# Kernel optimization log

Hardware: AMD Instinct MI355X
Metric: run time of the kernel (lower is better)

## Reference

```python
import jax, jax.numpy as jnp
import numpy as np
import math

D_MODEL = 1024
N_HEAD = 16
D_FF = 4096
N_LAYERS = 4
SEQ = 2048
BATCH = 1
LN_EPS = 1e-5


def _pos_encoding(S, D, dtype):
    pos = jnp.arange(S, dtype=dtype)[:, None]                      # [S,1]
    div = jnp.exp(jnp.arange(0, D, 2, dtype=dtype) * (-math.log(10000.0) / D))
    ang = pos * div                                                 # [S,D/2]
    pe = jnp.stack([jnp.sin(ang), jnp.cos(ang)], axis=-1).reshape(S, D)  # interleave sin/cos
    return pe[:, None, :]                                           # [S,1,D]


def _layernorm(x, g, b):
    mu = jnp.mean(x, axis=-1, keepdims=True)
    var = jnp.mean(jnp.square(x - mu), axis=-1, keepdims=True)
    return (x - mu) * jax.lax.rsqrt(var + LN_EPS) * g + b


def setup_inputs() -> dict:
    key = jax.random.key(0)
    ks = jax.random.split(key, 16)
    f32 = jnp.float32
    L, D, F = N_LAYERS, D_MODEL, D_FF
    s = 0.02
    inp = {
        "X": jax.random.normal(ks[0], (SEQ, BATCH, D), dtype=f32),
        "Wqkv": jax.random.normal(ks[1], (L, 3 * D, D), dtype=f32) * s,
        "bqkv": jnp.zeros((L, 3 * D), dtype=f32),
        "Wo": jax.random.normal(ks[2], (L, D, D), dtype=f32) * s,
        "bo": jnp.zeros((L, D), dtype=f32),
        "ln1_g": jnp.ones((L, D), dtype=f32),
        "ln1_b": jnp.zeros((L, D), dtype=f32),
        "W1": jax.random.normal(ks[3], (L, F, D), dtype=f32) * s,
        "b1": jnp.zeros((L, F), dtype=f32),
        "W2": jax.random.normal(ks[4], (L, D, F), dtype=f32) * s,
        "b2": jnp.zeros((L, D), dtype=f32),
        "ln2_g": jnp.ones((L, D), dtype=f32),
        "ln2_b": jnp.zeros((L, D), dtype=f32),
        "Wdec": jax.random.normal(ks[5], (3, D), dtype=f32) * s,
        "bdec": jnp.zeros((3,), dtype=f32),
        "window_size": 128,
        "nhead": 16,
    }
    return inp


def reference(X, Wqkv, bqkv, Wo, bo, ln1_g, ln1_b, W1, b1, W2, b2, ln2_g, ln2_b, Wdec, bdec, window_size, nhead):
    S, B, D = X.shape
    H = nhead
    hd = D // H
    scale = 1.0 / math.sqrt(hd)

    x = X + _pos_encoding(S, D, X.dtype)  # dropout is identity at eval

    # banded additive mask: allowed iff |i-j| < window_size (triu/tril(-inf) construction)
    idx = jnp.arange(S)
    band = jnp.abs(idx[:, None] - idx[None, :]) < window_size
    mask = jnp.where(band, jnp.array(0.0, X.dtype), jnp.array(-jnp.inf, X.dtype))  # [S,S]

    L = Wqkv.shape[0]
    for l in range(L):
        # self-attention (post-norm encoder layer)
        qkv = jnp.einsum('sbd,ed->sbe', x, Wqkv[l]) + bqkv[l]
        q, k, v = jnp.split(qkv, 3, axis=-1)
        q = q.reshape(S, B, H, hd)
        k = k.reshape(S, B, H, hd)
        v = v.reshape(S, B, H, hd)
        scores = jnp.einsum('sbhd,tbhd->bhst', q, k) * scale + mask  # [B,H,S,S]
        attn = jax.nn.softmax(scores, axis=-1)
        o = jnp.einsum('bhst,tbhd->sbhd', attn, v).reshape(S, B, D)
        o = jnp.einsum('sbd,ed->sbe', o, Wo[l]) + bo[l]
        x = _layernorm(x + o, ln1_g[l], ln1_b[l])
        # feed-forward (relu)
        h = jax.nn.relu(jnp.einsum('sbd,fd->sbf', x, W1[l]) + b1[l])
        ff = jnp.einsum('sbf,df->sbd', h, W2[l]) + b2[l]
        x = _layernorm(x + ff, ln2_g[l], ln2_b[l])

    logits = jnp.einsum('sbd,cd->sbc', x, Wdec) + bdec  # [S,B,3]
    return jax.nn.log_softmax(logits, axis=-1)
```

## Files before the change

kernel.cpp:

```cpp
#include <hip/hip_runtime.h>
#include <hip/hip_bf16.h>
#include <cmath>

typedef __hip_bfloat16 bf16;
typedef __bf16 bf16x8 __attribute__((ext_vector_type(8)));
typedef float f32x4 __attribute__((ext_vector_type(4)));

typedef __attribute__((address_space(1))) void void_g;
typedef __attribute__((address_space(3))) void void_l;

#define SEQ 2048
#define DMODEL 1024
#define NHEAD 16
#define HDIM 64
#define DFF 4096
#define WINDOW 128
#define LN_EPS 1e-5f

__device__ __forceinline__ void gl_lds16(const bf16* g, bf16* l) {
    __builtin_amdgcn_global_load_lds((void_g*)(g), (void_l*)(l), 16, 0, 0);
}

__device__ __forceinline__ bf16x8 cvt8(float4 a, float4 b) {
    bf16x8 w;
    w[0] = (__bf16)a.x; w[1] = (__bf16)a.y; w[2] = (__bf16)a.z; w[3] = (__bf16)a.w;
    w[4] = (__bf16)b.x; w[5] = (__bf16)b.y; w[6] = (__bf16)b.z; w[7] = (__bf16)b.w;
    return w;
}

__global__ __launch_bounds__(256)
void add_pe(const float* __restrict__ X, bf16* __restrict__ x) {
    int idx = blockIdx.x * 256 + threadIdx.x;
    int s = idx >> 10, d = idx & 1023;
    float i2 = (float)(d & ~1);
    float div = expf(i2 * (-9.210340371976184f / 1024.0f));
    float ang = (float)s * div;
    float pe = (d & 1) ? cosf(ang) : sinf(ang);
    x[idx] = (bf16)(X[idx] + pe);
}

__global__ __launch_bounds__(256)
void cvt_w_layer(const float* __restrict__ wqkv, const float* __restrict__ wo,
                 const float* __restrict__ w1, const float* __restrict__ w2,
                 bf16* __restrict__ dst)
{
    int i = blockIdx.x * 256 + threadIdx.x;
    const float* src; size_t so;
    if (i < 393216)       { src = wqkv; so = (size_t)i * 8; }
    else if (i < 524288)  { src = wo;   so = (size_t)(i - 393216) * 8; }
    else if (i < 1048576) { src = w1;   so = (size_t)(i - 524288) * 8; }
    else                  { src = w2;   so = (size_t)(i - 1048576) * 8; }
    float4 a = *(const float4*)(src + so);
    float4 b = *(const float4*)(src + so + 4);
    *(bf16x8*)(dst + (size_t)i * 8) = cvt8(a, b);
}


#define G8_PROLOGUE(Adecl, Wdecl)                                                \
    __shared__ __align__(16) bf16 AS[3][256 * 64];                               \
    __shared__ __align__(16) bf16 BS[3][128 * 64];                               \
    const int tid  = threadIdx.x;                                                \
    const int lane = tid & 63;                                                   \
    const int wave = tid >> 6;                                                   \
    const int wm = wave >> 1, wn = wave & 1;                                     \
    const int r = lane & 15, quad = lane >> 4;                                   \
    const int rc = (quad ^ (r & 3)) * 8;                                         \
    f32x4 acc[4][4];                                                             \
    _Pragma("unroll")                                                            \
    for (int i = 0; i < 4; ++i)                                                  \
        _Pragma("unroll")                                                        \
        for (int j = 0; j < 4; ++j) acc[i][j] = (f32x4){0.f, 0.f, 0.f, 0.f};     \
    const bf16* ApA[4]; const bf16* ApB[2];                                      \
    _Pragma("unroll")                                                            \
    for (int i = 0; i < 4; ++i) {                                                \
        int c = tid + 512 * i;                                                   \
        int ks = c >> 10, row = (c >> 2) & 255, kch = (c & 3) ^ (row & 3);       \
        ApA[i] = (Adecl) + (size_t)(m0 + row) * K + ks * 32 + kch * 8;           \
    }                                                                            \
    _Pragma("unroll")                                                            \
    for (int i = 0; i < 2; ++i) {                                                \
        int c = tid + 512 * i;                                                   \
        int ks = c >> 9, row = (c >> 2) & 127, kch = (c & 3) ^ (row & 3);        \
        ApB[i] = (Wdecl) + (size_t)(n0 + row) * K + ks * 32 + kch * 8;           \
    }

#define G8_STAGE(koff, Adst, Bdst)                                               \
    _Pragma("unroll")                                                            \
    for (int i = 0; i < 4; ++i)                                                  \
        gl_lds16(ApA[i] + (koff), (Adst) + (size_t)(tid + 512 * i) * 8);         \
    _Pragma("unroll")                                                            \
    for (int i = 0; i < 2; ++i)                                                  \
        gl_lds16(ApB[i] + (koff), (Bdst) + (size_t)(tid + 512 * i) * 8);

#define G8_KLOOP(Klim)                                                           \
    const int nit = (Klim) / 64;                                                 \
    bf16 *A_c = &AS[0][0], *A_n = &AS[1][0], *A_f = &AS[2][0];                   \
    bf16 *B_c = &BS[0][0], *B_n = &BS[1][0], *B_f = &BS[2][0];                   \
    G8_STAGE(0, A_c, B_c)                                                        \
    if (nit > 1) {                                                               \
        G8_STAGE(64, A_n, B_n)                                                   \
        asm volatile("s_waitcnt vmcnt(6)" ::: "memory");                         \
    } else {                                                                     \
        asm volatile("s_waitcnt vmcnt(0)" ::: "memory");                         \
    }                                                                            \
    __builtin_amdgcn_s_barrier();                                                \
    for (int t = 0; t < nit; ++t) {                                              \
        const bool stg = (t + 2 < nit);                                          \
        if (stg) { G8_STAGE((t + 2) * 64, A_f, B_f) }                            \
        bf16x8 av[4][2], bv[4][2];                                               \
        _Pragma("unroll")                                                        \
        for (int mf = 0; mf < 4; ++mf)                                           \
            _Pragma("unroll")                                                    \
            for (int kk = 0; kk < 2; ++kk)                                       \
                av[mf][kk] = *(const bf16x8*)(A_c + kk * 8192 +                  \
                              (wm * 64 + mf * 16 + r) * 32 + rc);                \
        _Pragma("unroll")                                                        \
        for (int nf = 0; nf < 4; ++nf)                                           \
            _Pragma("unroll")                                                    \
            for (int kk = 0; kk < 2; ++kk)                                       \
                bv[nf][kk] = *(const bf16x8*)(B_c + kk * 4096 +                  \
                              (wn * 64 + nf * 16 + r) * 32 + rc);                \
        __builtin_amdgcn_s_setprio(1);                                           \
        _Pragma("unroll")                                                        \
        for (int mf = 0; mf < 4; ++mf)                                           \
            _Pragma("unroll")                                                    \
            for (int nf = 0; nf < 4; ++nf)                                       \
                _Pragma("unroll")                                                \
                for (int kk = 0; kk < 2; ++kk)                                   \
                    acc[mf][nf] = __builtin_amdgcn_mfma_f32_16x16x32_bf16(       \
                        av[mf][kk], bv[nf][kk], acc[mf][nf], 0, 0, 0);           \
        __builtin_amdgcn_s_setprio(0);                                           \
        if (stg) asm volatile("s_waitcnt vmcnt(6)" ::: "memory");                \
        else     asm volatile("s_waitcnt vmcnt(0)" ::: "memory");                \
        __builtin_amdgcn_s_barrier();                                            \
        bf16* tA = A_c; A_c = A_n; A_n = A_f; A_f = tA;                          \
        bf16* tB = B_c; B_c = B_n; B_n = B_f; B_f = tB;                          \
    }

#define G8_SWZ_TILE()                                                            \
    const int gx = gridDim.x, gy = gridDim.y;                                    \
    const int bid = blockIdx.y * gx + blockIdx.x;                                \
    const int cpx = (gx * gy) >> 3;                                              \
    const int swz = (bid & 7) * cpx + (bid >> 3);                                \
    const int m0 = (swz / gx) * 256, n0 = (swz % gx) * 128;

template<int ACT>
__global__ __launch_bounds__(512)
void gemm8_bt(const bf16* __restrict__ A, const bf16* __restrict__ W,
              const float* __restrict__ bias, bf16* __restrict__ C,
              int M, int N, int K)
{
    G8_SWZ_TILE()
    G8_PROLOGUE(A, W)
    G8_KLOOP(K)
#pragma unroll
    for (int nt = 0; nt < 4; ++nt) {
        int n = n0 + wn * 64 + nt * 16 + r;
        float bv = bias[n];
#pragma unroll
        for (int mt = 0; mt < 4; ++mt) {
#pragma unroll
            for (int e = 0; e < 4; ++e) {
                int m = m0 + wm * 64 + mt * 16 + quad * 4 + e;
                float v = acc[mt][nt][e] + bv;
                if (ACT == 1) v = fmaxf(v, 0.f);
                C[(size_t)m * N + n] = (bf16)v;
            }
        }
    }
}

template<int SPLIT>
__global__ __launch_bounds__(512)
void gemm8_splitk(const bf16* __restrict__ A, const bf16* __restrict__ Wfull,
                  float* __restrict__ Cacc, int M, int N, int K)
{
    G8_SWZ_TILE()
    const int Kc = K / SPLIT;
    const bf16* Ab = A + (size_t)blockIdx.z * Kc;
    const bf16* W = Wfull + (size_t)blockIdx.z * Kc;
    float* Cz = Cacc + (size_t)blockIdx.z * M * N;
    G8_PROLOGUE(Ab, W)
    G8_KLOOP(Kc)
#pragma unroll
    for (int nt = 0; nt < 4; ++nt) {
        int n = n0 + wn * 64 + nt * 16 + r;
#pragma unroll
        for (int mt = 0; mt < 4; ++mt) {
#pragma unroll
            for (int e = 0; e < 4; ++e) {
                int m = m0 + wm * 64 + mt * 16 + quad * 4 + e;
                Cz[(size_t)m * N + n] = acc[mt][nt][e];
            }
        }
    }
}

__global__ __launch_bounds__(256)
void transpose_v(const bf16* __restrict__ qkv, bf16* __restrict__ Vt)
{
    __shared__ __bf16 t[64][66];
    const int s0 = blockIdx.x * 64, dm0 = blockIdx.y * 64;
    const int tid = threadIdx.x;
    const int sl = tid >> 2, dc = (tid & 3) * 16;
    const bf16* src = qkv + (size_t)(s0 + sl) * 3072 + 2048 + dm0 + dc;
    bf16x8 v0 = *(const bf16x8*)(src);
    bf16x8 v1 = *(const bf16x8*)(src + 8);
#pragma unroll
    for (int j = 0; j < 8; ++j) { t[sl][dc + j] = v0[j]; t[sl][dc + 8 + j] = v1[j]; }
    __syncthreads();
    const int dl = tid >> 2, sc = (tid & 3) * 16;
    bf16x8 o0, o1;
#pragma unroll
    for (int j = 0; j < 8; ++j) { o0[j] = t[sc + j][dl]; o1[j] = t[sc + 8 + j][dl]; }
    bf16* dst = Vt + (size_t)(dm0 + dl) * SEQ + s0 + sc;
    *(bf16x8*)(dst) = o0;
    *(bf16x8*)(dst + 8) = o1;
}

__global__ __launch_bounds__(256)
void attn_mfma(const bf16* __restrict__ qkv, const bf16* __restrict__ Vt,
               bf16* __restrict__ o)
{
    __shared__ __align__(16) __bf16 Plds[4][16 * 40];
    const int tid = threadIdx.x, lane = tid & 63, w = tid >> 6;
    const int h = blockIdx.x & 15;
    const int qw = (blockIdx.x >> 4) * 64 + w * 16;
    const int r = lane & 15, quad = lane >> 4;
    __bf16* P = Plds[w];

    bf16x8 qa[2];
    {
        const bf16* qrow = qkv + (size_t)(qw + r) * 3072 + h * 64 + quad * 8;
#pragma unroll
        for (int c = 0; c < 2; ++c) {
            bf16x8 t = *(const bf16x8*)(qrow + c * 32);
#pragma unroll
            for (int j = 0; j < 8; ++j) qa[c][j] = (__bf16)((float)t[j] * 0.125f);
        }
    }

    bf16x8 ones;
#pragma unroll
    for (int j = 0; j < 8; ++j) ones[j] = (__bf16)1.0f;

    f32x4 acc[4];
#pragma unroll
    for (int d = 0; d < 4; ++d) acc[d] = (f32x4){0.f, 0.f, 0.f, 0.f};
    float m_run[4], l_run[4];
#pragma unroll
    for (int e = 0; e < 4; ++e) { m_run[e] = -1e30f; l_run[e] = 0.f; }

    int jmin = qw - (WINDOW - 1); if (jmin < 0) jmin = 0;
    int jmax = qw + 15 + (WINDOW - 1); if (jmax > SEQ - 1) jmax = SEQ - 1;

    for (int kt = jmin & ~31; kt <= jmax; kt += 32) {
        f32x4 S[2];
#pragma unroll
        for (int c = 0; c < 2; ++c) {
            const bf16* krow = qkv + (size_t)(kt + 16 * c + r) * 3072 + 1024 + h * 64 + quad * 8;
            bf16x8 kb0 = *(const bf16x8*)(krow);
            bf16x8 kb1 = *(const bf16x8*)(krow + 32);
            f32x4 s = (f32x4){0.f, 0.f, 0.f, 0.f};
            s = __builtin_amdgcn_mfma_f32_16x16x32_bf16(qa[0], kb0, s, 0, 0, 0);
            s = __builtin_amdgcn_mfma_f32_16x16x32_bf16(qa[1], kb1, s, 0, 0, 0);
            S[c] = s;
        }
#pragma unroll
        for (int c = 0; c < 2; ++c)
#pragma unroll
            for (int e = 0; e < 4; ++e) {
                int j = kt + 16 * c + r;
                int i = qw + quad * 4 + e;
                bool valid = (unsigned)(j - i + (WINDOW - 1)) <= (unsigned)(2 * WINDOW - 2);
                S[c][e] = valid ? S[c][e] : -1e30f;
            }
        float alpha[4], mnew[4];
#pragma unroll
        for (int e = 0; e < 4; ++e) {
            float v = fmaxf(S[0][e], S[1][e]);
#pragma unroll
            for (int off = 1; off <= 8; off <<= 1) v = fmaxf(v, __shfl_xor(v, off, 64));
            mnew[e] = fmaxf(m_run[e], v);
            alpha[e] = __expf(m_run[e] - mnew[e]);
            m_run[e] = mnew[e];
        }
#pragma unroll
        for (int c = 0; c < 2; ++c)
#pragma unroll
            for (int e = 0; e < 4; ++e) {
                float p = __expf(S[c][e] - mnew[e]);
                p = (S[c][e] <= -1e29f) ? 0.f : p;
                P[(quad * 4 + e) * 40 + 16 * c + r] = (__bf16)p;
            }
        bf16x8 pa = *(const bf16x8*)(P + r * 40 + quad * 8);
#pragma unroll
        for (int d = 0; d < 4; ++d)
#pragma unroll
            for (int e = 0; e < 4; ++e) acc[d][e] *= alpha[e];
        f32x4 ls = (f32x4){0.f, 0.f, 0.f, 0.f};
        ls = __builtin_amdgcn_mfma_f32_16x16x32_bf16(pa, ones, ls, 0, 0, 0);
#pragma unroll
        for (int e = 0; e < 4; ++e) l_run[e] = l_run[e] * alpha[e] + ls[e];
#pragma unroll
        for (int d = 0; d < 4; ++d) {
            const bf16* vrow = Vt + (size_t)(h * 64 + 16 * d + r) * SEQ + kt + quad * 8;
            bf16x8 vb = *(const bf16x8*)(vrow);
            acc[d] = __builtin_amdgcn_mfma_f32_16x16x32_bf16(pa, vb, acc[d], 0, 0, 0);
        }
    }

#pragma unroll
    for (int d = 0; d < 4; ++d)
#pragma unroll
        for (int e = 0; e < 4; ++e) {
            int i = qw + quad * 4 + e;
            o[(size_t)i * DMODEL + h * 64 + 16 * d + r] = (bf16)(acc[d][e] / l_run[e]);
        }
}

__global__ __launch_bounds__(256)
void ln_residual_f32(bf16* __restrict__ x, const float* __restrict__ accd,
                     const float* __restrict__ bias,
                     const float* __restrict__ gamma, const float* __restrict__ beta)
{
    const int s = blockIdx.x, tid = threadIdx.x;
    const int lane = tid & 63, wave = tid >> 6;
    __shared__ float red[8];
    float v[4];
    float sum = 0.f;
#pragma unroll
    for (int i = 0; i < 4; ++i) {
        int d = i * 256 + tid;
        float a = accd[(size_t)s * 1024 + d]
                + accd[(size_t)SEQ * 1024 + (size_t)s * 1024 + d]
                + accd[2 * (size_t)SEQ * 1024 + (size_t)s * 1024 + d]
                + accd[3 * (size_t)SEQ * 1024 + (size_t)s * 1024 + d];
        v[i] = (float)x[(size_t)s * 1024 + d] + a + bias[d];
        sum += v[i];
    }
#pragma unroll
    for (int off = 32; off; off >>= 1) sum += __shfl_xor(sum, off, 64);
    if (lane == 0) red[wave] = sum;
    __syncthreads();
    float mu = (red[0] + red[1] + red[2] + red[3]) * (1.f / 1024.f);
    float sq = 0.f;
#pragma unroll
    for (int i = 0; i < 4; ++i) { float t = v[i] - mu; sq += t * t; }
#pragma unroll
    for (int off = 32; off; off >>= 1) sq += __shfl_xor(sq, off, 64);
    if (lane == 0) red[wave + 4] = sq;
    __syncthreads();
    float var = (red[4] + red[5] + red[6] + red[7]) * (1.f / 1024.f);
    float inv = rsqrtf(var + LN_EPS);
#pragma unroll
    for (int i = 0; i < 4; ++i) {
        int d = i * 256 + tid;
        x[(size_t)s * 1024 + d] = (bf16)((v[i] - mu) * inv * gamma[d] + beta[d]);
    }
}

__global__ __launch_bounds__(256)
void decoder(const bf16* __restrict__ x, const float* __restrict__ Wdec,
             const float* __restrict__ bdec, float* __restrict__ out)
{
    const int s = blockIdx.x * 4 + (threadIdx.x >> 6);
    const int lane = threadIdx.x & 63;
    float a0 = 0.f, a1 = 0.f, a2 = 0.f;
    for (int d = lane; d < 1024; d += 64) {
        float xv = (float)x[(size_t)s * 1024 + d];
        a0 += xv * Wdec[d];
        a1 += xv * Wdec[1024 + d];
        a2 += xv * Wdec[2048 + d];
    }
#pragma unroll
    for (int off = 32; off; off >>= 1) {
        a0 += __shfl_xor(a0, off, 64);
        a1 += __shfl_xor(a1, off, 64);
        a2 += __shfl_xor(a2, off, 64);
    }
    if (lane == 0) {
        float z0 = a0 + bdec[0];
        float z1 = a1 + bdec[1];
        float z2 = a2 + bdec[2];
        float mx = fmaxf(z0, fmaxf(z1, z2));
        float lse = mx + logf(__expf(z0 - mx) + __expf(z1 - mx) + __expf(z2 - mx));
        out[s * 3 + 0] = z0 - lse;
        out[s * 3 + 1] = z1 - lse;
        out[s * 3 + 2] = z2 - lse;
    }
}

extern "C" void kernel_launch(void* const* d_in, const int* in_sizes, int n_in,
                              void* d_out, int out_size, void* d_ws, size_t ws_size,
                              hipStream_t stream)
{
    const float* X    = (const float*)d_in[0];
    const float* Wqkv = (const float*)d_in[1];
    const float* bqkv = (const float*)d_in[2];
    const float* Wo   = (const float*)d_in[3];
    const float* bo   = (const float*)d_in[4];
    const float* ln1g = (const float*)d_in[5];
    const float* ln1b = (const float*)d_in[6];
    const float* W1   = (const float*)d_in[7];
    const float* b1   = (const float*)d_in[8];
    const float* W2   = (const float*)d_in[9];
    const float* b2   = (const float*)d_in[10];
    const float* ln2g = (const float*)d_in[11];
    const float* ln2b = (const float*)d_in[12];
    const float* Wdec = (const float*)d_in[13];
    const float* bdec = (const float*)d_in[14];

    bf16* ws   = (bf16*)d_ws;
    bf16* x    = ws;
    bf16* buf  = x   + (size_t)SEQ * DMODEL;
    bf16* qkv  = buf;
    bf16* ao   = buf + (size_t)SEQ * 3 * DMODEL;
    bf16* h    = buf;
    bf16* Vt   = buf + (size_t)SEQ * DFF;
    float* accf = (float*)(Vt + (size_t)SEQ * DMODEL);
    bf16* Wb   = (bf16*)(accf + 4 * (size_t)SEQ * DMODEL);
    bf16* WoB  = Wb + 3145728;
    bf16* W1B  = Wb + 4194304;
    bf16* W2B  = Wb + 8388608;

    add_pe<<<(SEQ * DMODEL) / 256, 256, 0, stream>>>(X, x);

    for (int l = 0; l < 4; ++l) {
        cvt_w_layer<<<6144, 256, 0, stream>>>(
            Wqkv + (size_t)l * 3145728, Wo + (size_t)l * 1048576,
            W1 + (size_t)l * 4194304,  W2 + (size_t)l * 4194304, Wb);
        gemm8_bt<0><<<dim3(3072 / 128, SEQ / 256), 512, 0, stream>>>(
            x, Wb, bqkv + l * 3072, qkv, SEQ, 3072, 1024);
        transpose_v<<<dim3(SEQ / 64, DMODEL / 64), 256, 0, stream>>>(qkv, Vt);
        attn_mfma<<<(SEQ / 64) * NHEAD, 256, 0, stream>>>(qkv, Vt, ao);
        gemm8_splitk<4><<<dim3(1024 / 128, SEQ / 256, 4), 512, 0, stream>>>(
            ao, WoB, accf, SEQ, 1024, 1024);
        ln_residual_f32<<<SEQ, 256, 0, stream>>>(x, accf, bo + l * 1024,
                                                 ln1g + l * 1024, ln1b + l * 1024);
        gemm8_bt<1><<<dim3(4096 / 128, SEQ / 256), 512, 0, stream>>>(
            x, W1B, b1 + l * 4096, h, SEQ, 4096, 1024);
        gemm8_splitk<4><<<dim3(1024 / 128, SEQ / 256, 4), 512, 0, stream>>>(
            h, W2B, accf, SEQ, 1024, 4096);
        ln_residual_f32<<<SEQ, 256, 0, stream>>>(x, accf, b2 + l * 1024,
                                                 ln2g + l * 1024, ln2b + l * 1024);
    }

    decoder<<<SEQ / 4, 256, 0, stream>>>(x, Wdec, bdec, (float*)d_out);
}
```

Baseline: 825.0 us.

## Fuse V transpose into QKV GEMM epilogue and use XCD-aware tile swizzles

The QKV GEMM now writes the V columns directly in transposed layout to Vt, so the separate transpose_v kernel launch and its extra read and write of V are gone. The block-to-tile mapping in both GEMM kernels is also replaced with XCD-aware grouping: blocks on the same XCD (bid mod 8) get a compact SXxSY patch of tiles, which should improve L2 reuse of A and W. The transposed V stores are 8-byte strided writes and may coalesce poorly. The new mapping depends on grid sizes dividing evenly by the template parameters.

```diff
diff --git a/kernel.cpp b/kernel.cpp
--- a/kernel.cpp
+++ b/kernel.cpp
@@ -4,6 +4,7 @@
 
 typedef __hip_bfloat16 bf16;
 typedef __bf16 bf16x8 __attribute__((ext_vector_type(8)));
+typedef __bf16 bf16x4 __attribute__((ext_vector_type(4)));
 typedef float f32x4 __attribute__((ext_vector_type(4)));
 
 typedef __attribute__((address_space(1))) void void_g;
@@ -137,49 +138,72 @@
         bf16* tB = B_c; B_c = B_n; B_n = B_f; B_f = tB;                          \
     }
 
-#define G8_SWZ_TILE()                                                            \
-    const int gx = gridDim.x, gy = gridDim.y;                                    \
-    const int bid = blockIdx.y * gx + blockIdx.x;                                \
-    const int cpx = (gx * gy) >> 3;                                              \
-    const int swz = (bid & 7) * cpx + (bid >> 3);                                \
-    const int m0 = (swz / gx) * 256, n0 = (swz % gx) * 128;
-
-template<int ACT>
+template<int ACT, int SX, int SY, int VOUT>
 __global__ __launch_bounds__(512)
 void gemm8_bt(const bf16* __restrict__ A, const bf16* __restrict__ W,
               const float* __restrict__ bias, bf16* __restrict__ C,
-              int M, int N, int K)
-{
-    G8_SWZ_TILE()
+              bf16* __restrict__ Vt, int M, int N, int K)
+{
+    const int gx = gridDim.x;
+    const int l = blockIdx.y * gx + blockIdx.x;
+    const int k = l & 7, j = l >> 3;
+    const int xg = gx / SX;
+    const int tx = (k % xg) * SX + (j % SX);
+    const int ty = (k / xg) * SY + (j / SX);
+    const int m0 = ty * 256, n0 = tx * 128;
     G8_PROLOGUE(A, W)
     G8_KLOOP(K)
-#pragma unroll
-    for (int nt = 0; nt < 4; ++nt) {
-        int n = n0 + wn * 64 + nt * 16 + r;
-        float bv = bias[n];
-#pragma unroll
-        for (int mt = 0; mt < 4; ++mt) {
-#pragma unroll
-            for (int e = 0; e < 4; ++e) {
-                int m = m0 + wm * 64 + mt * 16 + quad * 4 + e;
-                float v = acc[mt][nt][e] + bv;
-                if (ACT == 1) v = fmaxf(v, 0.f);
-                C[(size_t)m * N + n] = (bf16)v;
+    if (VOUT && n0 >= 2048) {
+#pragma unroll
+        for (int nt = 0; nt < 4; ++nt) {
+            int n = n0 + wn * 64 + nt * 16 + r;
+            float bv = bias[n];
+            int dv = n - 2048;
+#pragma unroll
+            for (int mt = 0; mt < 4; ++mt) {
+                int m = m0 + wm * 64 + mt * 16 + quad * 4;
+                bf16x4 pk;
+#pragma unroll
+                for (int e = 0; e < 4; ++e) pk[e] = (__bf16)(acc[mt][nt][e] + bv);
+                *(bf16x4*)(Vt + (size_t)dv * SEQ + m) = pk;
             }
         }
-    }
-}
-
-template<int SPLIT>
+    } else {
+#pragma unroll
+        for (int nt = 0; nt < 4; ++nt) {
+            int n = n0 + wn * 64 + nt * 16 + r;
+            float bv = bias[n];
+#pragma unroll
+            for (int mt = 0; mt < 4; ++mt) {
+#pragma unroll
+                for (int e = 0; e < 4; ++e) {
+                    int m = m0 + wm * 64 + mt * 16 + quad * 4 + e;
+                    float v = acc[mt][nt][e] + bv;
+                    if (ACT == 1) v = fmaxf(v, 0.f);
+                    C[(size_t)m * N + n] = (bf16)v;
+                }
+            }
+        }
+    }
+}
+
+template<int SPLIT, int SY>
 __global__ __launch_bounds__(512)
 void gemm8_splitk(const bf16* __restrict__ A, const bf16* __restrict__ Wfull,
                   float* __restrict__ Cacc, int M, int N, int K)
 {
-    G8_SWZ_TILE()
+    const int gx = gridDim.x, gy = gridDim.y;
+    const int l = (blockIdx.z * gy + blockIdx.y) * gx + blockIdx.x;
+    const int k = l & 7, j = l >> 3;
+    const int yg = gy / SY;
+    const int tx = j % gx;
+    const int ty = (k % yg) * SY + (j / gx);
+    const int tz = k / yg;
+    const int m0 = ty * 256, n0 = tx * 128;
     const int Kc = K / SPLIT;
-    const bf16* Ab = A + (size_t)blockIdx.z * Kc;
-    const bf16* W = Wfull + (size_t)blockIdx.z * Kc;
-    float* Cz = Cacc + (size_t)blockIdx.z * M * N;
+    const bf16* Ab = A + (size_t)tz * Kc;
+    const bf16* W = Wfull + (size_t)tz * Kc;
+    float* Cz = Cacc + (size_t)tz * M * N;
     G8_PROLOGUE(Ab, W)
     G8_KLOOP(Kc)
 #pragma unroll
@@ -194,28 +218,6 @@
             }
         }
     }
-}
-
-__global__ __launch_bounds__(256)
-void transpose_v(const bf16* __restrict__ qkv, bf16* __restrict__ Vt)
-{
-    __shared__ __bf16 t[64][66];
-    const int s0 = blockIdx.x * 64, dm0 = blockIdx.y * 64;
-    const int tid = threadIdx.x;
-    const int sl = tid >> 2, dc = (tid & 3) * 16;
-    const bf16* src = qkv + (size_t)(s0 + sl) * 3072 + 2048 + dm0 + dc;
-    bf16x8 v0 = *(const bf16x8*)(src);
-    bf16x8 v1 = *(const bf16x8*)(src + 8);
-#pragma unroll
-    for (int j = 0; j < 8; ++j) { t[sl][dc + j] = v0[j]; t[sl][dc + 8 + j] = v1[j]; }
-    __syncthreads();
-    const int dl = tid >> 2, sc = (tid & 3) * 16;
-    bf16x8 o0, o1;
-#pragma unroll
-    for (int j = 0; j < 8; ++j) { o0[j] = t[sc + j][dl]; o1[j] = t[sc + 8 + j][dl]; }
-    bf16* dst = Vt + (size_t)(dm0 + dl) * SEQ + s0 + sc;
-    *(bf16x8*)(dst) = o0;
-    *(bf16x8*)(dst + 8) = o1;
 }
 
 __global__ __launch_bounds__(256)
@@ -430,17 +432,16 @@
         cvt_w_layer<<<6144, 256, 0, stream>>>(
             Wqkv + (size_t)l * 3145728, Wo + (size_t)l * 1048576,
             W1 + (size_t)l * 4194304,  W2 + (size_t)l * 4194304, Wb);
-        gemm8_bt<0><<<dim3(3072 / 128, SEQ / 256), 512, 0, stream>>>(
-            x, Wb, bqkv + l * 3072, qkv, SEQ, 3072, 1024);
-        transpose_v<<<dim3(SEQ / 64, DMODEL / 64), 256, 0, stream>>>(qkv, Vt);
+        gemm8_bt<0, 6, 4, 1><<<dim3(3072 / 128, SEQ / 256), 512, 0, stream>>>(
+            x, Wb, bqkv + l * 3072, qkv, Vt, SEQ, 3072, 1024);
         attn_mfma<<<(SEQ / 64) * NHEAD, 256, 0, stream>>>(qkv, Vt, ao);
-        gemm8_splitk<4><<<dim3(1024 / 128, SEQ / 256, 4), 512, 0, stream>>>(
+        gemm8_splitk<4, 4><<<dim3(1024 / 128, SEQ / 256, 4), 512, 0, stream>>>(
             ao, WoB, accf, SEQ, 1024, 1024);
         ln_residual_f32<<<SEQ, 256, 0, stream>>>(x, accf, bo + l * 1024,
                                                  ln1g + l * 1024, ln1b + l * 1024);
-        gemm8_bt<1><<<dim3(4096 / 128, SEQ / 256), 512, 0, stream>>>(
-            x, W1B, b1 + l * 4096, h, SEQ, 4096, 1024);
-        gemm8_splitk<4><<<dim3(1024 / 128, SEQ / 256, 4), 512, 0, stream>>>(
+        gemm8_bt<1, 8, 4, 0><<<dim3(4096 / 128, SEQ / 256), 512, 0, stream>>>(
+            x, W1B, b1 + l * 4096, h, nullptr, SEQ, 4096, 1024);
+        gemm8_splitk<4, 4><<<dim3(1024 / 128, SEQ / 256, 4), 512, 0, stream>>>(
             h, W2B, accf, SEQ, 1024, 4096);
         ln_residual_f32<<<SEQ, 256, 0, stream>>>(x, accf, b2 + l * 1024,
                                                  ln2g + l * 1024, ln2b + l * 1024);
```

After: 811.2 us. No clear change (-1.7%).
